# Optimization experiments

Measured on AMD Instinct MI355X. Metric: run time of the kernel, lower is better.

Reference implementation:

```python
import jax, jax.numpy as jnp
import numpy as np

N = 16384
IN_F = 256
OUT_F = 128
ALPHA = 0.2  # leaky relu negative slope
NEG = -9e15


def _xavier(key, shape, gain=1.414):
    fan_in, fan_out = shape
    a = gain * np.sqrt(6.0 / (fan_in + fan_out))
    return jax.random.uniform(key, shape, jnp.float32, -a, a)


def setup_inputs() -> dict:
    key = jax.random.key(0)
    k_h, k_adj, k_q, k_k, k_v = jax.random.split(key, 5)
    h = jax.random.normal(k_h, (N, IN_F), dtype=jnp.float32)
    adj = jax.random.randint(k_adj, (N, N), 0, 2, dtype=jnp.int32)
    W_query = _xavier(k_q, (IN_F, OUT_F))
    W_key = _xavier(k_k, (IN_F, OUT_F))
    W_value = _xavier(k_v, (IN_F, OUT_F))
    return {"h": h, "adj": adj, "W_query": W_query, "W_key": W_key, "W_value": W_value}


def reference(h, adj, W_query, W_key, W_value):
    # h: [N, in], adj: [N, N] 0/1
    Q = h @ W_query           # [N, out]
    K = h @ W_key             # [N, out]
    V = h @ W_value           # [N, out]
    e = jnp.einsum('nd,md->nm', Q, K)          # [N, N]
    e = jnp.where(e >= 0, e, ALPHA * e)         # leaky relu
    e = jnp.where(adj > 0, e, NEG)              # adjacency mask
    attention = jax.nn.softmax(e, axis=1)       # row softmax
    # dropout: eval mode (training=False) -> identity
    h_prime = attention @ V                     # [N, out]
    return jax.nn.elu(h_prime)                  # concat=True
```

## Files before the change

kernel.cpp:

```cpp
#include <hip/hip_runtime.h>

#define N_TOK 16384
#define ALPHA_LRELU 0.2f
#define NEGV -9e15f
#define NSPLIT 3
#define LOG2E 1.44269504f
#define DEFER_THR 8.0f

typedef _Float16 f16;
typedef __attribute__((ext_vector_type(8))) _Float16 f16x8;
typedef __attribute__((ext_vector_type(4))) float f32x4;
typedef __attribute__((ext_vector_type(4))) int i32x4;
typedef unsigned short u16;

__device__ __forceinline__ float bf2f(u16 b) {
  unsigned u = ((unsigned)b) << 16;
  return __builtin_bit_cast(float, u);
}
__device__ __forceinline__ f16x8 cvt8(i32x4 v) {
  f16x8 r;
#pragma unroll
  for (int i = 0; i < 4; ++i) {
    unsigned u = __builtin_bit_cast(unsigned, v[i]);
    r[2 * i]     = (f16)__builtin_bit_cast(float, (u & 0xffffu) << 16);
    r[2 * i + 1] = (f16)__builtin_bit_cast(float, u & 0xffff0000u);
  }
  return r;
}

__global__ __launch_bounds__(64) void detect_kernel(const u16* __restrict__ h16,
                                                    int* __restrict__ flag)
{
  int lane = threadIdx.x;
  unsigned u = h16[lane * 2];
  unsigned e = (u >> 7) & 0xFFu;
  int sane = (e >= 0x60u && e <= 0x8Eu) ? 1 : 0;
#pragma unroll
  for (int off = 32; off >= 1; off >>= 1) sane += __shfl_xor(sane, off);
  if (lane == 0) *flag = (sane >= 32) ? 1 : 0;
}

__global__ __launch_bounds__(256) void sentinel_kernel(float* __restrict__ out) {
  int i = blockIdx.x * 256 + threadIdx.x;
  if (i < N_TOK * 128) out[i] = 100.0f;
}

__global__ __launch_bounds__(256) void wt_kernel(
    const int* __restrict__ flag,
    const void* __restrict__ Wq, const void* __restrict__ Wk,
    const void* __restrict__ Wv, f16* __restrict__ Wt)
{
  const int isbf = *flag;
  int w = blockIdx.y;
  const void* W = (w == 0) ? Wq : (w == 1) ? Wk : Wv;
  int idx = blockIdx.x * 256 + threadIdx.x;
  int k = idx >> 7, n = idx & 127;
  float v = isbf ? bf2f(((const u16*)W)[idx]) : ((const float*)W)[idx];
  if (w == 0) v *= LOG2E;
  Wt[w * 32768 + n * 256 + k] = (f16)v;
}

__global__ __launch_bounds__(256) void qkv_kernel(
    const int* __restrict__ flag, const void* __restrict__ hvp,
    const f16* __restrict__ Wt,
    f16* __restrict__ Qo, f16* __restrict__ Ko, f16* __restrict__ Vt)
{
  const int isbf = *flag;
  const int mb = blockIdx.x * 64;
  const int gy = blockIdx.y;
  const int tid = threadIdx.x;
  const int wave = tid >> 6, lane = tid & 63, quad = lane >> 4, l16 = lane & 15;

  __shared__ __align__(16) f16 hs[64][256 + 8];

  if (isbf) {
    const u16* h = (const u16*)hvp;
#pragma unroll
    for (int i = 0; i < 8; ++i) {
      int c = i * 256 + tid;
      int r = c >> 5, o = c & 31;
      i32x4 v = *(const i32x4*)(h + (size_t)(mb + r) * 256 + o * 8);
      *(f16x8*)(&hs[r][o * 8]) = cvt8(v);
    }
  } else {
    const float* h = (const float*)hvp;
#pragma unroll
    for (int i = 0; i < 8; ++i) {
      int c = i * 256 + tid;
      int r = c >> 5, o = c & 31;
      const float* p = h + (size_t)(mb + r) * 256 + o * 8;
      f32x4 v0 = *(const f32x4*)p, v1 = *(const f32x4*)(p + 4);
      f16x8 q;
#pragma unroll
      for (int j = 0; j < 4; ++j) { q[j] = (f16)v0[j]; q[4 + j] = (f16)v1[j]; }
      *(f16x8*)(&hs[r][o * 8]) = q;
    }
  }
  __syncthreads();

  const f16* Wg = Wt + gy * 32768;

  if (gy < 2) {
    f16x8 a[8];
#pragma unroll
    for (int ks = 0; ks < 8; ++ks)
      a[ks] = *(const f16x8*)(&hs[wave * 16 + l16][ks * 32 + quad * 8]);
    f32x4 acc[8];
#pragma unroll
    for (int ct = 0; ct < 8; ++ct) acc[ct] = (f32x4){0.f, 0.f, 0.f, 0.f};
#pragma unroll
    for (int ks = 0; ks < 8; ++ks)
#pragma unroll
      for (int ct = 0; ct < 8; ++ct) {
        f16x8 b = *(const f16x8*)(Wg + (ct * 16 + l16) * 256 + ks * 32 + quad * 8);
        acc[ct] = __builtin_amdgcn_mfma_f32_16x16x32_f16(a[ks], b, acc[ct], 0, 0, 0);
      }
    f16* O = (gy == 0) ? Qo : Ko;
#pragma unroll
    for (int ct = 0; ct < 8; ++ct)
#pragma unroll
      for (int r = 0; r < 4; ++r)
        O[(size_t)(mb + wave * 16 + quad * 4 + r) * 128 + ct * 16 + l16] = (f16)acc[ct][r];
  } else {
    f32x4 acc[2][4];
#pragma unroll
    for (int ft = 0; ft < 2; ++ft)
#pragma unroll
      for (int bt = 0; bt < 4; ++bt) acc[ft][bt] = (f32x4){0.f, 0.f, 0.f, 0.f};
#pragma unroll
    for (int ks = 0; ks < 8; ++ks) {
      f16x8 a2[2], b2[4];
#pragma unroll
      for (int ft = 0; ft < 2; ++ft)
        a2[ft] = *(const f16x8*)(Wg + ((wave * 2 + ft) * 16 + l16) * 256 + ks * 32 + quad * 8);
#pragma unroll
      for (int bt = 0; bt < 4; ++bt)
        b2[bt] = *(const f16x8*)(&hs[bt * 16 + l16][ks * 32 + quad * 8]);
#pragma unroll
      for (int ft = 0; ft < 2; ++ft)
#pragma unroll
        for (int bt = 0; bt < 4; ++bt)
          acc[ft][bt] = __builtin_amdgcn_mfma_f32_16x16x32_f16(a2[ft], b2[bt], acc[ft][bt], 0, 0, 0);
    }
#pragma unroll
    for (int ft = 0; ft < 2; ++ft)
#pragma unroll
      for (int bt = 0; bt < 4; ++bt)
#pragma unroll
        for (int r = 0; r < 4; ++r)
          Vt[(size_t)((wave * 2 + ft) * 16 + quad * 4 + r) * N_TOK + mb + bt * 16 + l16] =
              (f16)acc[ft][bt][r];
  }
}

__global__ __launch_bounds__(256, 2) void flash_kernel(
    const f16* __restrict__ Q, const f16* __restrict__ Kg,
    const f16* __restrict__ Vt, const int* __restrict__ adj,
    float* __restrict__ Opart, float* __restrict__ mpart,
    float* __restrict__ lpart)
{
  const int qb = blockIdx.x * 64;
  const int ksec = blockIdx.y;
  const int base = 256 / NSPLIT;
  const int rem  = 256 % NSPLIT;
  const int iters = base + (ksec < rem ? 1 : 0);
  const int tile0 = ksec * base + (ksec < rem ? ksec : rem);
  const int kb0 = tile0 * 64;
  const int tid = threadIdx.x;
  const int wave = tid >> 6, lane = tid & 63, quad = lane >> 4, l16 = lane & 15;

  __shared__ __align__(16) f16 Ks[2][64][136];
  __shared__ __align__(16) f16 Vs[2][128][72];
  __shared__ __align__(16) f16 Ps[4][16][72];

  f16x8 qf[4];
#pragma unroll
  for (int ks = 0; ks < 4; ++ks)
    qf[ks] = *(const f16x8*)(Q + (size_t)(qb + wave * 16 + l16) * 128 + ks * 32 + quad * 8);

  f16x8 ONES;
#pragma unroll
  for (int j = 0; j < 8; ++j) ONES[j] = (f16)1.0f;

  const int* aprow[4];
#pragma unroll
  for (int r = 0; r < 4; ++r)
    aprow[r] = adj + (size_t)(qb + wave * 16 + quad * 4 + r) * N_TOK + l16;

  f32x4 Oacc[8];
#pragma unroll
  for (int ot = 0; ot < 8; ++ot) Oacc[ot] = (f32x4){0.f, 0.f, 0.f, 0.f};
  f32x4 Lacc = (f32x4){0.f, 0.f, 0.f, 0.f};
  float m2[4];
#pragma unroll
  for (int r = 0; r < 4; ++r) m2[r] = -INFINITY;

  i32x4 pK[4], pV[4];
  int am[4][4];

#pragma unroll
  for (int i = 0; i < 4; ++i) {
    int c = i * 256 + tid;
    pK[i] = *(const i32x4*)(Kg + (size_t)(kb0 + (c >> 4)) * 128 + (c & 15) * 8);
    pV[i] = *(const i32x4*)(Vt + (size_t)(c >> 3) * N_TOK + kb0 + (c & 7) * 8);
  }
#pragma unroll
  for (int r = 0; r < 4; ++r)
#pragma unroll
    for (int ct = 0; ct < 4; ++ct)
      am[r][ct] = aprow[r][kb0 + ct * 16];
#pragma unroll
  for (int i = 0; i < 4; ++i) {
    int c = i * 256 + tid;
    *(f16x8*)(&Ks[0][c >> 4][(c & 15) * 8]) = __builtin_bit_cast(f16x8, pK[i]);
    *(f16x8*)(&Vs[0][c >> 3][(c & 7) * 8])  = __builtin_bit_cast(f16x8, pV[i]);
  }
  if (iters > 1) {
    int kb = kb0 + 64;
#pragma unroll
    for (int i = 0; i < 4; ++i) {
      int c = i * 256 + tid;
      pK[i] = *(const i32x4*)(Kg + (size_t)(kb + (c >> 4)) * 128 + (c & 15) * 8);
      pV[i] = *(const i32x4*)(Vt + (size_t)(c >> 3) * N_TOK + kb + (c & 7) * 8);
    }
  }
  __syncthreads();

  for (int it = 0; it < iters; ++it) {
    const int cur = it & 1;
    const int nxt = cur ^ 1;

    if (it + 1 < iters) {
#pragma unroll
      for (int i = 0; i < 4; ++i) {
        int c = i * 256 + tid;
        *(f16x8*)(&Ks[nxt][c >> 4][(c & 15) * 8]) = __builtin_bit_cast(f16x8, pK[i]);
        *(f16x8*)(&Vs[nxt][c >> 3][(c & 7) * 8])  = __builtin_bit_cast(f16x8, pV[i]);
      }
    }
    if (it + 2 < iters) {
      int kb = kb0 + (it + 2) * 64;
#pragma unroll
      for (int i = 0; i < 4; ++i) {
        int c = i * 256 + tid;
        pK[i] = *(const i32x4*)(Kg + (size_t)(kb + (c >> 4)) * 128 + (c & 15) * 8);
        pV[i] = *(const i32x4*)(Vt + (size_t)(c >> 3) * N_TOK + kb + (c & 7) * 8);
      }
    }

    float sc[4][4];
#pragma unroll
    for (int ct = 0; ct < 4; ++ct) {
      f32x4 s = (f32x4){0.f, 0.f, 0.f, 0.f};
#pragma unroll
      for (int ks = 0; ks < 4; ++ks) {
        f16x8 b = *(const f16x8*)(&Ks[cur][ct * 16 + l16][ks * 32 + quad * 8]);
        s = __builtin_amdgcn_mfma_f32_16x16x32_f16(qf[ks], b, s, 0, 0, 0);
      }
#pragma unroll
      for (int r = 0; r < 4; ++r) {
        float v = s[r];
        v = fmaxf(v, ALPHA_LRELU * v);
        sc[ct][r] = (am[r][ct] > 0) ? v : NEGV;
      }
    }
    if (it + 1 < iters) {
      int kb = kb0 + (it + 1) * 64;
#pragma unroll
      for (int r = 0; r < 4; ++r)
#pragma unroll
        for (int ct = 0; ct < 4; ++ct)
          am[r][ct] = aprow[r][kb + ct * 16];
    }

    float mx[4];
#pragma unroll
    for (int r = 0; r < 4; ++r) {
      float m = fmaxf(fmaxf(sc[0][r], sc[1][r]), fmaxf(sc[2][r], sc[3][r]));
#pragma unroll
      for (int off = 8; off >= 1; off >>= 1)
        m = fmaxf(m, __shfl_xor(m, off, 16));
      mx[r] = m;
    }
    bool up = (mx[0] > m2[0] + DEFER_THR) | (mx[1] > m2[1] + DEFER_THR) |
              (mx[2] > m2[2] + DEFER_THR) | (mx[3] > m2[3] + DEFER_THR);
    if (__ballot(up)) {
      float al[4];
#pragma unroll
      for (int r = 0; r < 4; ++r) {
        float mn = fmaxf(m2[r], mx[r]);
        al[r] = exp2f(m2[r] - mn);
        m2[r] = mn;
      }
#pragma unroll
      for (int ot = 0; ot < 8; ++ot)
#pragma unroll
        for (int r = 0; r < 4; ++r) Oacc[ot][r] *= al[r];
#pragma unroll
      for (int r = 0; r < 4; ++r) Lacc[r] *= al[r];
    }

#pragma unroll
    for (int ct = 0; ct < 4; ++ct)
#pragma unroll
      for (int r = 0; r < 4; ++r)
        Ps[wave][quad * 4 + r][ct * 16 + l16] = (f16)exp2f(sc[ct][r] - m2[r]);

    asm volatile("s_waitcnt lgkmcnt(0)" ::: "memory");
    f16x8 pa0 = *(const f16x8*)(&Ps[wave][l16][quad * 8]);
    f16x8 pa1 = *(const f16x8*)(&Ps[wave][l16][32 + quad * 8]);
#pragma unroll
    for (int ot = 0; ot < 8; ++ot) {
      f16x8 b0 = *(const f16x8*)(&Vs[cur][ot * 16 + l16][quad * 8]);
      f16x8 b1 = *(const f16x8*)(&Vs[cur][ot * 16 + l16][32 + quad * 8]);
      Oacc[ot] = __builtin_amdgcn_mfma_f32_16x16x32_f16(pa0, b0, Oacc[ot], 0, 0, 0);
      Oacc[ot] = __builtin_amdgcn_mfma_f32_16x16x32_f16(pa1, b1, Oacc[ot], 0, 0, 0);
    }
    Lacc = __builtin_amdgcn_mfma_f32_16x16x32_f16(pa0, ONES, Lacc, 0, 0, 0);
    Lacc = __builtin_amdgcn_mfma_f32_16x16x32_f16(pa1, ONES, Lacc, 0, 0, 0);

    __syncthreads();
  }

  float* Op = Opart + (size_t)ksec * (N_TOK * 128);
#pragma unroll
  for (int ot = 0; ot < 8; ++ot)
#pragma unroll
    for (int r = 0; r < 4; ++r) {
      int row = qb + wave * 16 + quad * 4 + r;
      Op[(size_t)row * 128 + ot * 16 + l16] = Oacc[ot][r];
    }
  if (l16 == 0) {
#pragma unroll
    for (int r = 0; r < 4; ++r) {
      int row = qb + wave * 16 + quad * 4 + r;
      mpart[ksec * N_TOK + row] = m2[r];
      lpart[ksec * N_TOK + row] = Lacc[r];
    }
  }
}

__global__ __launch_bounds__(256) void combine_kernel(
    const float* __restrict__ Opart, const float* __restrict__ mpart,
    const float* __restrict__ lpart, float* __restrict__ out)
{
  const int qb = blockIdx.x * 64;
  const int t = threadIdx.x;
  __shared__ float sa[NSPLIT][64], sdn[64];
  if (t < 64) {
    float m = -INFINITY;
#pragma unroll
    for (int s = 0; s < NSPLIT; ++s) m = fmaxf(m, mpart[s * N_TOK + qb + t]);
    float dn = 0.f;
#pragma unroll
    for (int s = 0; s < NSPLIT; ++s) {
      float a = exp2f(mpart[s * N_TOK + qb + t] - m);
      sa[s][t] = a;
      dn += lpart[s * N_TOK + qb + t] * a;
    }
    sdn[t] = 1.0f / dn;
  }
  __syncthreads();
  float* Og = out + (size_t)qb * 128;
#pragma unroll
  for (int i = 0; i < 8; ++i) {
    int idx = (i * 256 + t) * 4;
    int row = idx >> 7;
    f32x4 acc = (f32x4){0.f, 0.f, 0.f, 0.f};
#pragma unroll
    for (int s = 0; s < NSPLIT; ++s) {
      f32x4 o = *(const f32x4*)(Opart + (size_t)s * (N_TOK * 128) + (size_t)qb * 128 + idx);
      float a = sa[s][row];
#pragma unroll
      for (int j = 0; j < 4; ++j) acc[j] += o[j] * a;
    }
    float dn = sdn[row];
    f32x4 v;
#pragma unroll
    for (int j = 0; j < 4; ++j) {
      float x = acc[j] * dn;
      v[j] = (x > 0.f) ? x : (__expf(x) - 1.f);
    }
    *(f32x4*)(Og + idx) = v;
  }
}

__global__ __launch_bounds__(256) void flash1_kernel(
    const f16* __restrict__ Q, const f16* __restrict__ Kg,
    const f16* __restrict__ Vt, const int* __restrict__ adj,
    float* __restrict__ out)
{
  const int qb = blockIdx.x * 64;
  const int tid = threadIdx.x;
  const int wave = tid >> 6, lane = tid & 63, quad = lane >> 4, l16 = lane & 15;

  __shared__ __align__(16) f16 Ks[64][136];
  __shared__ __align__(16) f16 Vs[128][72];
  __shared__ __align__(16) int As[64][68];
  __shared__ __align__(16) f16 Ps[4][16][72];

  f16x8 qf[4];
#pragma unroll
  for (int ks = 0; ks < 4; ++ks)
    qf[ks] = *(const f16x8*)(Q + (size_t)(qb + wave * 16 + l16) * 128 + ks * 32 + quad * 8);
  f16x8 ONES;
#pragma unroll
  for (int j = 0; j < 8; ++j) ONES[j] = (f16)1.0f;

  f32x4 Oacc[8];
#pragma unroll
  for (int ot = 0; ot < 8; ++ot) Oacc[ot] = (f32x4){0.f, 0.f, 0.f, 0.f};
  f32x4 Lacc = (f32x4){0.f, 0.f, 0.f, 0.f};
  float m2[4];
#pragma unroll
  for (int r = 0; r < 4; ++r) m2[r] = -INFINITY;

  i32x4 pK[4], pV[4], pA[4];
#pragma unroll
  for (int i = 0; i < 4; ++i) {
    int c = i * 256 + tid;
    pK[i] = *(const i32x4*)(Kg + (size_t)(c >> 4) * 128 + (c & 15) * 8);
    pV[i] = *(const i32x4*)(Vt + (size_t)(c >> 3) * N_TOK + (c & 7) * 8);
    pA[i] = *(const i32x4*)(adj + (size_t)(qb + (c >> 4)) * N_TOK + (c & 15) * 4);
  }

  for (int it = 0; it < 256; ++it) {
    __syncthreads();
#pragma unroll
    for (int i = 0; i < 4; ++i) {
      int c = i * 256 + tid;
      *(f16x8*)(&Ks[c >> 4][(c & 15) * 8]) = __builtin_bit_cast(f16x8, pK[i]);
      *(f16x8*)(&Vs[c >> 3][(c & 7) * 8])  = __builtin_bit_cast(f16x8, pV[i]);
      *(i32x4*)(&As[c >> 4][(c & 15) * 4]) = pA[i];
    }
    __syncthreads();
    if (it + 1 < 256) {
      int kb = (it + 1) * 64;
#pragma unroll
      for (int i = 0; i < 4; ++i) {
        int c = i * 256 + tid;
        pK[i] = *(const i32x4*)(Kg + (size_t)(kb + (c >> 4)) * 128 + (c & 15) * 8);
        pV[i] = *(const i32x4*)(Vt + (size_t)(c >> 3) * N_TOK + kb + (c & 7) * 8);
        pA[i] = *(const i32x4*)(adj + (size_t)(qb + (c >> 4)) * N_TOK + kb + (c & 15) * 4);
      }
    }
    float sc[4][4];
#pragma unroll
    for (int ct = 0; ct < 4; ++ct) {
      f32x4 s = (f32x4){0.f, 0.f, 0.f, 0.f};
#pragma unroll
      for (int ks = 0; ks < 4; ++ks) {
        f16x8 b = *(const f16x8*)(&Ks[ct * 16 + l16][ks * 32 + quad * 8]);
        s = __builtin_amdgcn_mfma_f32_16x16x32_f16(qf[ks], b, s, 0, 0, 0);
      }
#pragma unroll
      for (int r = 0; r < 4; ++r) {
        float v = s[r];
        v = fmaxf(v, ALPHA_LRELU * v);
        sc[ct][r] = (As[wave * 16 + quad * 4 + r][ct * 16 + l16] > 0) ? v : NEGV;
      }
    }
    float mx[4];
#pragma unroll
    for (int r = 0; r < 4; ++r) {
      float m = fmaxf(fmaxf(sc[0][r], sc[1][r]), fmaxf(sc[2][r], sc[3][r]));
#pragma unroll
      for (int off = 8; off >= 1; off >>= 1)
        m = fmaxf(m, __shfl_xor(m, off, 16));
      mx[r] = m;
    }
    bool up = (mx[0] > m2[0] + DEFER_THR) | (mx[1] > m2[1] + DEFER_THR) |
              (mx[2] > m2[2] + DEFER_THR) | (mx[3] > m2[3] + DEFER_THR);
    if (__ballot(up)) {
      float al[4];
#pragma unroll
      for (int r = 0; r < 4; ++r) {
        float mn = fmaxf(m2[r], mx[r]);
        al[r] = exp2f(m2[r] - mn);
        m2[r] = mn;
      }
#pragma unroll
      for (int ot = 0; ot < 8; ++ot)
#pragma unroll
        for (int r = 0; r < 4; ++r) Oacc[ot][r] *= al[r];
#pragma unroll
      for (int r = 0; r < 4; ++r) Lacc[r] *= al[r];
    }
#pragma unroll
    for (int ct = 0; ct < 4; ++ct)
#pragma unroll
      for (int r = 0; r < 4; ++r)
        Ps[wave][quad * 4 + r][ct * 16 + l16] = (f16)exp2f(sc[ct][r] - m2[r]);

    asm volatile("s_waitcnt lgkmcnt(0)" ::: "memory");
    f16x8 pa0 = *(const f16x8*)(&Ps[wave][l16][quad * 8]);
    f16x8 pa1 = *(const f16x8*)(&Ps[wave][l16][32 + quad * 8]);
#pragma unroll
    for (int ot = 0; ot < 8; ++ot) {
      f16x8 b0 = *(const f16x8*)(&Vs[ot * 16 + l16][quad * 8]);
      f16x8 b1 = *(const f16x8*)(&Vs[ot * 16 + l16][32 + quad * 8]);
      Oacc[ot] = __builtin_amdgcn_mfma_f32_16x16x32_f16(pa0, b0, Oacc[ot], 0, 0, 0);
      Oacc[ot] = __builtin_amdgcn_mfma_f32_16x16x32_f16(pa1, b1, Oacc[ot], 0, 0, 0);
    }
    Lacc = __builtin_amdgcn_mfma_f32_16x16x32_f16(pa0, ONES, Lacc, 0, 0, 0);
    Lacc = __builtin_amdgcn_mfma_f32_16x16x32_f16(pa1, ONES, Lacc, 0, 0, 0);
  }
#pragma unroll
  for (int ot = 0; ot < 8; ++ot)
#pragma unroll
    for (int r = 0; r < 4; ++r) {
      float v = Oacc[ot][r] / Lacc[r];
      v = (v > 0.f) ? v : (__expf(v) - 1.f);
      int row = qb + wave * 16 + quad * 4 + r;
      out[(size_t)row * 128 + ot * 16 + l16] = v;
    }
}

extern "C" void kernel_launch(void* const* d_in, const int* in_sizes, int n_in,
                              void* d_out, int out_size, void* d_ws, size_t ws_size,
                              hipStream_t stream)
{
  const void* h  = d_in[0];
  const int* adj = (const int*)d_in[1];
  const void* Wq = d_in[2];
  const void* Wk = d_in[3];
  const void* Wv = d_in[4];
  float* out = (float*)d_out;

  char* ws = (char*)d_ws;
  int* flag = (int*)ws;
  f16* Wt = (f16*)(ws + 1024);
  f16* Q  = (f16*)(ws + 262144);
  f16* K  = (f16*)(ws + 4456448);
  f16* Vt = (f16*)(ws + 8650752);
  float* Opart = (float*)(ws + 12845056);
  float* mpart = (float*)(ws + 38010880);
  float* lpart = (float*)(ws + 38207488);
  const size_t NEED_BASE  = 12845056;
  const size_t NEED_SPLIT = 38404096;

  if (ws_size < NEED_BASE) {
    sentinel_kernel<<<(N_TOK * 128 + 255) / 256, 256, 0, stream>>>(out);
    return;
  }

  detect_kernel<<<1, 64, 0, stream>>>((const u16*)h, flag);
  wt_kernel<<<dim3(128, 3), 256, 0, stream>>>(flag, Wq, Wk, Wv, Wt);
  qkv_kernel<<<dim3(256, 3), 256, 0, stream>>>(flag, h, Wt, Q, K, Vt);

  if (ws_size >= NEED_SPLIT) {
    flash_kernel<<<dim3(256, NSPLIT), 256, 0, stream>>>(Q, K, Vt, adj,
                                                        Opart, mpart, lpart);
    combine_kernel<<<dim3(256), 256, 0, stream>>>(Opart, mpart, lpart, out);
  } else {
    flash1_kernel<<<dim3(256), 256, 0, stream>>>(Q, K, Vt, adj, out);
  }
}
```

Baseline: 1.537 ms.

## Process two 16-row query tiles per wave and split keys four ways

Each wave now handles 32 query rows (two 16-row groups) against every K/V tile staged in shared memory. This halves K/V global and LDS traffic per query row and computes S transposed so each lane holds one query row. The adjacency mask is packed into bitmasks, and its loads are split so they interleave with the two PV passes. The key split goes from 3 to 4, giving 128x4 blocks with more accumulator registers per thread, which risks lower occupancy or spills.

```diff
diff --git a/kernel.cpp b/kernel.cpp
--- a/kernel.cpp
+++ b/kernel.cpp
@@ -3,11 +3,12 @@
 #define N_TOK 16384
 #define ALPHA_LRELU 0.2f
 #define NEGV -9e15f
-#define NSPLIT 3
+#define NSPLIT 4
 #define LOG2E 1.44269504f
 #define DEFER_THR 8.0f
 
 typedef _Float16 f16;
+typedef __attribute__((ext_vector_type(4))) _Float16 f16x4;
 typedef __attribute__((ext_vector_type(8))) _Float16 f16x8;
 typedef __attribute__((ext_vector_type(4))) float f32x4;
 typedef __attribute__((ext_vector_type(4))) int i32x4;
@@ -159,13 +160,10 @@
     float* __restrict__ Opart, float* __restrict__ mpart,
     float* __restrict__ lpart)
 {
-  const int qb = blockIdx.x * 64;
+  const int qb = blockIdx.x * 128;
   const int ksec = blockIdx.y;
-  const int base = 256 / NSPLIT;
-  const int rem  = 256 % NSPLIT;
-  const int iters = base + (ksec < rem ? 1 : 0);
-  const int tile0 = ksec * base + (ksec < rem ? ksec : rem);
-  const int kb0 = tile0 * 64;
+  const int iters = 256 / NSPLIT;
+  const int kb0 = ksec * iters * 64;
   const int tid = threadIdx.x;
   const int wave = tid >> 6, lane = tid & 63, quad = lane >> 4, l16 = lane & 15;
 
@@ -173,30 +171,33 @@
   __shared__ __align__(16) f16 Vs[2][128][72];
   __shared__ __align__(16) f16 Ps[4][16][72];
 
-  f16x8 qf[4];
-#pragma unroll
-  for (int ks = 0; ks < 4; ++ks)
-    qf[ks] = *(const f16x8*)(Q + (size_t)(qb + wave * 16 + l16) * 128 + ks * 32 + quad * 8);
+  f16x8 qfA[4], qfB[4];
+  const f16* qp = Q + (size_t)(qb + wave * 32 + l16) * 128;
+#pragma unroll
+  for (int ks = 0; ks < 4; ++ks) {
+    qfA[ks] = *(const f16x8*)(qp + ks * 32 + quad * 8);
+    qfB[ks] = *(const f16x8*)(qp + 16 * 128 + ks * 32 + quad * 8);
+  }
 
   f16x8 ONES;
 #pragma unroll
   for (int j = 0; j < 8; ++j) ONES[j] = (f16)1.0f;
 
-  const int* aprow[4];
-#pragma unroll
-  for (int r = 0; r < 4; ++r)
-    aprow[r] = adj + (size_t)(qb + wave * 16 + quad * 4 + r) * N_TOK + l16;
-
-  f32x4 Oacc[8];
-#pragma unroll
-  for (int ot = 0; ot < 8; ++ot) Oacc[ot] = (f32x4){0.f, 0.f, 0.f, 0.f};
-  f32x4 Lacc = (f32x4){0.f, 0.f, 0.f, 0.f};
-  float m2[4];
-#pragma unroll
-  for (int r = 0; r < 4; ++r) m2[r] = -INFINITY;
+  const int* aprA = adj + (size_t)(qb + wave * 32 + l16) * N_TOK;
+  const int* aprB = aprA + (size_t)16 * N_TOK;
+
+  f32x4 OA[8], OB[8];
+#pragma unroll
+  for (int ot = 0; ot < 8; ++ot) {
+    OA[ot] = (f32x4){0.f, 0.f, 0.f, 0.f};
+    OB[ot] = (f32x4){0.f, 0.f, 0.f, 0.f};
+  }
+  f32x4 LA = (f32x4){0.f, 0.f, 0.f, 0.f};
+  f32x4 LB = (f32x4){0.f, 0.f, 0.f, 0.f};
+  float mA = -INFINITY, mB = -INFINITY;
 
   i32x4 pK[4], pV[4];
-  int am[4][4];
+  unsigned amA, amB;
 
 #pragma unroll
   for (int i = 0; i < 4; ++i) {
@@ -204,11 +205,18 @@
     pK[i] = *(const i32x4*)(Kg + (size_t)(kb0 + (c >> 4)) * 128 + (c & 15) * 8);
     pV[i] = *(const i32x4*)(Vt + (size_t)(c >> 3) * N_TOK + kb0 + (c & 7) * 8);
   }
-#pragma unroll
-  for (int r = 0; r < 4; ++r)
+  {
+    unsigned a0 = 0, b0 = 0;
 #pragma unroll
     for (int ct = 0; ct < 4; ++ct)
-      am[r][ct] = aprow[r][kb0 + ct * 16];
+#pragma unroll
+      for (int r = 0; r < 4; ++r) {
+        int col = kb0 + ct * 16 + quad * 4 + r;
+        a0 |= (unsigned)(aprA[col] > 0) << (ct * 4 + r);
+        b0 |= (unsigned)(aprB[col] > 0) << (ct * 4 + r);
+      }
+    amA = a0; amB = b0;
+  }
 #pragma unroll
   for (int i = 0; i < 4; ++i) {
     int c = i * 256 + tid;
@@ -229,6 +237,7 @@
   for (int it = 0; it < iters; ++it) {
     const int cur = it & 1;
     const int nxt = cur ^ 1;
+    const int kbn = kb0 + (it + 1) * 64;
 
     if (it + 1 < iters) {
 #pragma unroll
@@ -248,94 +257,160 @@
       }
     }
 
-    float sc[4][4];
+    f32x4 sA[4], sB[4];
 #pragma unroll
     for (int ct = 0; ct < 4; ++ct) {
-      f32x4 s = (f32x4){0.f, 0.f, 0.f, 0.f};
+      sA[ct] = (f32x4){0.f, 0.f, 0.f, 0.f};
+      sB[ct] = (f32x4){0.f, 0.f, 0.f, 0.f};
+    }
+#pragma unroll
+    for (int ct = 0; ct < 4; ++ct)
 #pragma unroll
       for (int ks = 0; ks < 4; ++ks) {
-        f16x8 b = *(const f16x8*)(&Ks[cur][ct * 16 + l16][ks * 32 + quad * 8]);
-        s = __builtin_amdgcn_mfma_f32_16x16x32_f16(qf[ks], b, s, 0, 0, 0);
-      }
+        f16x8 a = *(const f16x8*)(&Ks[cur][ct * 16 + l16][ks * 32 + quad * 8]);
+        sA[ct] = __builtin_amdgcn_mfma_f32_16x16x32_f16(a, qfA[ks], sA[ct], 0, 0, 0);
+        sB[ct] = __builtin_amdgcn_mfma_f32_16x16x32_f16(a, qfB[ks], sB[ct], 0, 0, 0);
+      }
+
+    float scA[4][4], scB[4][4];
+#pragma unroll
+    for (int ct = 0; ct < 4; ++ct)
 #pragma unroll
       for (int r = 0; r < 4; ++r) {
-        float v = s[r];
-        v = fmaxf(v, ALPHA_LRELU * v);
-        sc[ct][r] = (am[r][ct] > 0) ? v : NEGV;
-      }
-    }
+        float vA = sA[ct][r];
+        vA = fmaxf(vA, ALPHA_LRELU * vA);
+        scA[ct][r] = ((amA >> (ct * 4 + r)) & 1u) ? vA : NEGV;
+        float vB = sB[ct][r];
+        vB = fmaxf(vB, ALPHA_LRELU * vB);
+        scB[ct][r] = ((amB >> (ct * 4 + r)) & 1u) ? vB : NEGV;
+      }
+
+    int tmA[16], tmB[16];
     if (it + 1 < iters) {
-      int kb = kb0 + (it + 1) * 64;
-#pragma unroll
-      for (int r = 0; r < 4; ++r)
-#pragma unroll
-        for (int ct = 0; ct < 4; ++ct)
-          am[r][ct] = aprow[r][kb + ct * 16];
-    }
-
-    float mx[4];
+#pragma unroll
+      for (int ct = 0; ct < 4; ++ct)
+#pragma unroll
+        for (int r = 0; r < 4; ++r)
+          tmA[ct * 4 + r] = aprA[kbn + ct * 16 + quad * 4 + r];
+    }
+
+    float mxA = scA[0][0], mxB = scB[0][0];
+#pragma unroll
+    for (int ct = 0; ct < 4; ++ct)
+#pragma unroll
+      for (int r = 0; r < 4; ++r) {
+        mxA = fmaxf(mxA, scA[ct][r]);
+        mxB = fmaxf(mxB, scB[ct][r]);
+      }
+    mxA = fmaxf(mxA, __shfl_xor(mxA, 16));
+    mxA = fmaxf(mxA, __shfl_xor(mxA, 32));
+    mxB = fmaxf(mxB, __shfl_xor(mxB, 16));
+    mxB = fmaxf(mxB, __shfl_xor(mxB, 32));
+
+    bool up = (mxA > mA + DEFER_THR) | (mxB > mB + DEFER_THR);
+    if (__ballot(up)) {
+      float mnA = fmaxf(mA, mxA), alA = exp2f(mA - mnA); mA = mnA;
+      float mnB = fmaxf(mB, mxB), alB = exp2f(mB - mnB); mB = mnB;
+      float aOA[4], aOB[4];
+#pragma unroll
+      for (int r = 0; r < 4; ++r) {
+        aOA[r] = __shfl(alA, quad * 4 + r);
+        aOB[r] = __shfl(alB, quad * 4 + r);
+      }
+#pragma unroll
+      for (int ot = 0; ot < 8; ++ot)
+#pragma unroll
+        for (int r = 0; r < 4; ++r) {
+          OA[ot][r] *= aOA[r];
+          OB[ot][r] *= aOB[r];
+        }
+#pragma unroll
+      for (int r = 0; r < 4; ++r) { LA[r] *= aOA[r]; LB[r] *= aOB[r]; }
+    }
+
+#pragma unroll
+    for (int ct = 0; ct < 4; ++ct) {
+      f16x4 pw;
+#pragma unroll
+      for (int r = 0; r < 4; ++r) pw[r] = (f16)exp2f(scA[ct][r] - mA);
+      *(f16x4*)(&Ps[wave][l16][ct * 16 + quad * 4]) = pw;
+    }
+    asm volatile("s_waitcnt lgkmcnt(0)" ::: "memory");
+    {
+      f16x8 pa0 = *(const f16x8*)(&Ps[wave][l16][quad * 8]);
+      f16x8 pa1 = *(const f16x8*)(&Ps[wave][l16][32 + quad * 8]);
+#pragma unroll
+      for (int ot = 0; ot < 8; ++ot) {
+        f16x8 b0 = *(const f16x8*)(&Vs[cur][ot * 16 + l16][quad * 8]);
+        f16x8 b1 = *(const f16x8*)(&Vs[cur][ot * 16 + l16][32 + quad * 8]);
+        OA[ot] = __builtin_amdgcn_mfma_f32_16x16x32_f16(pa0, b0, OA[ot], 0, 0, 0);
+        OA[ot] = __builtin_amdgcn_mfma_f32_16x16x32_f16(pa1, b1, OA[ot], 0, 0, 0);
+      }
+      LA = __builtin_amdgcn_mfma_f32_16x16x32_f16(pa0, ONES, LA, 0, 0, 0);
+      LA = __builtin_amdgcn_mfma_f32_16x16x32_f16(pa1, ONES, LA, 0, 0, 0);
+    }
+
+    if (it + 1 < iters) {
+#pragma unroll
+      for (int ct = 0; ct < 4; ++ct)
+#pragma unroll
+        for (int r = 0; r < 4; ++r)
+          tmB[ct * 4 + r] = aprB[kbn + ct * 16 + quad * 4 + r];
+    }
+
+#pragma unroll
+    for (int ct = 0; ct < 4; ++ct) {
+      f16x4 pw;
+#pragma unroll
+      for (int r = 0; r < 4; ++r) pw[r] = (f16)exp2f(scB[ct][r] - mB);
+      *(f16x4*)(&Ps[wave][l16][ct * 16 + quad * 4]) = pw;
+    }
+    asm volatile("s_waitcnt lgkmcnt(0)" ::: "memory");
+    {
+      f16x8 pa0 = *(const f16x8*)(&Ps[wave][l16][quad * 8]);
+      f16x8 pa1 = *(const f16x8*)(&Ps[wave][l16][32 + quad * 8]);
+#pragma unroll
+      for (int ot = 0; ot < 8; ++ot) {
+        f16x8 b0 = *(const f16x8*)(&Vs[cur][ot * 16 + l16][quad * 8]);
+        f16x8 b1 = *(const f16x8*)(&Vs[cur][ot * 16 + l16][32 + quad * 8]);
+        OB[ot] = __builtin_amdgcn_mfma_f32_16x16x32_f16(pa0, b0, OB[ot], 0, 0, 0);
+        OB[ot] = __builtin_amdgcn_mfma_f32_16x16x32_f16(pa1, b1, OB[ot], 0, 0, 0);
+      }
+      LB = __builtin_amdgcn_mfma_f32_16x16x32_f16(pa0, ONES, LB, 0, 0, 0);
+      LB = __builtin_amdgcn_mfma_f32_16x16x32_f16(pa1, ONES, LB, 0, 0, 0);
+    }
+
+    if (it + 1 < iters) {
+      unsigned a0 = 0, b0 = 0;
+#pragma unroll
+      for (int j = 0; j < 16; ++j) {
+        a0 |= (unsigned)(tmA[j] > 0) << j;
+        b0 |= (unsigned)(tmB[j] > 0) << j;
+      }
+      amA = a0; amB = b0;
+    }
+
+    __syncthreads();
+  }
+
+  float* Op = Opart + (size_t)ksec * (N_TOK * 128);
+#pragma unroll
+  for (int ot = 0; ot < 8; ++ot)
 #pragma unroll
     for (int r = 0; r < 4; ++r) {
-      float m = fmaxf(fmaxf(sc[0][r], sc[1][r]), fmaxf(sc[2][r], sc[3][r]));
-#pragma unroll
-      for (int off = 8; off >= 1; off >>= 1)
-        m = fmaxf(m, __shfl_xor(m, off, 16));
-      mx[r] = m;
-    }
-    bool up = (mx[0] > m2[0] + DEFER_THR) | (mx[1] > m2[1] + DEFER_THR) |
-              (mx[2] > m2[2] + DEFER_THR) | (mx[3] > m2[3] + DEFER_THR);
-    if (__ballot(up)) {
-      float al[4];
-#pragma unroll
-      for (int r = 0; r < 4; ++r) {
-        float mn = fmaxf(m2[r], mx[r]);
-        al[r] = exp2f(m2[r] - mn);
-        m2[r] = mn;
-      }
-#pragma unroll
-      for (int ot = 0; ot < 8; ++ot)
-#pragma unroll
-        for (int r = 0; r < 4; ++r) Oacc[ot][r] *= al[r];
-#pragma unroll
-      for (int r = 0; r < 4; ++r) Lacc[r] *= al[r];
-    }
-
-#pragma unroll
-    for (int ct = 0; ct < 4; ++ct)
-#pragma unroll
-      for (int r = 0; r < 4; ++r)
-        Ps[wave][quad * 4 + r][ct * 16 + l16] = (f16)exp2f(sc[ct][r] - m2[r]);
-
-    asm volatile("s_waitcnt lgkmcnt(0)" ::: "memory");
-    f16x8 pa0 = *(const f16x8*)(&Ps[wave][l16][quad * 8]);
-    f16x8 pa1 = *(const f16x8*)(&Ps[wave][l16][32 + quad * 8]);
-#pragma unroll
-    for (int ot = 0; ot < 8; ++ot) {
-      f16x8 b0 = *(const f16x8*)(&Vs[cur][ot * 16 + l16][quad * 8]);
-      f16x8 b1 = *(const f16x8*)(&Vs[cur][ot * 16 + l16][32 + quad * 8]);
-      Oacc[ot] = __builtin_amdgcn_mfma_f32_16x16x32_f16(pa0, b0, Oacc[ot], 0, 0, 0);
-      Oacc[ot] = __builtin_amdgcn_mfma_f32_16x16x32_f16(pa1, b1, Oacc[ot], 0, 0, 0);
-    }
-    Lacc = __builtin_amdgcn_mfma_f32_16x16x32_f16(pa0, ONES, Lacc, 0, 0, 0);
-    Lacc = __builtin_amdgcn_mfma_f32_16x16x32_f16(pa1, ONES, Lacc, 0, 0, 0);
-
-    __syncthreads();
-  }
-
-  float* Op = Opart + (size_t)ksec * (N_TOK * 128);
-#pragma unroll
-  for (int ot = 0; ot < 8; ++ot)
+      int rowA = qb + wave * 32 + quad * 4 + r;
+      Op[(size_t)rowA * 128 + ot * 16 + l16] = OA[ot][r];
+      Op[(size_t)(rowA + 16) * 128 + ot * 16 + l16] = OB[ot][r];
+    }
+  if (quad == 0) {
+    mpart[ksec * N_TOK + qb + wave * 32 + l16] = mA;
+    mpart[ksec * N_TOK + qb + wave * 32 + 16 + l16] = mB;
+  }
+  if (l16 == 0) {
 #pragma unroll
     for (int r = 0; r < 4; ++r) {
-      int row = qb + wave * 16 + quad * 4 + r;
-      Op[(size_t)row * 128 + ot * 16 + l16] = Oacc[ot][r];
-    }
-  if (l16 == 0) {
-#pragma unroll
-    for (int r = 0; r < 4; ++r) {
-      int row = qb + wave * 16 + quad * 4 + r;
-      mpart[ksec * N_TOK + row] = m2[r];
-      lpart[ksec * N_TOK + row] = Lacc[r];
+      lpart[ksec * N_TOK + qb + wave * 32 + quad * 4 + r] = LA[r];
+      lpart[ksec * N_TOK + qb + wave * 32 + 16 + quad * 4 + r] = LB[r];
     }
   }
 }
@@ -534,10 +609,10 @@
   f16* K  = (f16*)(ws + 4456448);
   f16* Vt = (f16*)(ws + 8650752);
   float* Opart = (float*)(ws + 12845056);
-  float* mpart = (float*)(ws + 38010880);
-  float* lpart = (float*)(ws + 38207488);
+  float* mpart = (float*)(ws + 46399488);
+  float* lpart = (float*)(ws + 46661632);
   const size_t NEED_BASE  = 12845056;
-  const size_t NEED_SPLIT = 38404096;
+  const size_t NEED_SPLIT = 46923776;
 
   if (ws_size < NEED_BASE) {
     sentinel_kernel<<<(N_TOK * 128 + 255) / 256, 256, 0, stream>>>(out);
@@ -549,7 +624,7 @@
   qkv_kernel<<<dim3(256, 3), 256, 0, stream>>>(flag, h, Wt, Q, K, Vt);
 
   if (ws_size >= NEED_SPLIT) {
-    flash_kernel<<<dim3(256, NSPLIT), 256, 0, stream>>>(Q, K, Vt, adj,
+    flash_kernel<<<dim3(128, NSPLIT), 256, 0, stream>>>(Q, K, Vt, adj,
                                                         Opart, mpart, lpart);
     combine_kernel<<<dim3(256), 256, 0, stream>>>(Opart, mpart, lpart, out);
   } else {
```

After: 1.531 ms. No clear change (-0.4%).

## Stage K/V tiles via direct global-to-LDS loads with XOR swizzle, single buffer

Applied to the files above, without the earlier changes.

Replaces register-staged double-buffered K/V tiles with global_load_lds direct-to-LDS transfers into a single buffer. Bank conflicts are avoided with an XOR swizzle instead of padding. The smaller LDS footprint and fewer registers allow raising the occupancy hint to 3 blocks per CU. The cost is that loads are no longer overlapped with compute inside a block: each iteration waits on vmcnt(0) with an extra barrier, so latency hiding depends on the other resident blocks.

```diff
diff --git a/kernel.cpp b/kernel.cpp
--- a/kernel.cpp
+++ b/kernel.cpp
@@ -26,6 +26,12 @@
     r[2 * i + 1] = (f16)__builtin_bit_cast(float, u & 0xffff0000u);
   }
   return r;
+}
+
+__device__ __forceinline__ void gload16(const void* g, void* l) {
+  __builtin_amdgcn_global_load_lds(
+      (const __attribute__((address_space(1))) unsigned*)g,
+      (__attribute__((address_space(3))) unsigned*)l, 16, 0, 0);
 }
 
 __global__ __launch_bounds__(64) void detect_kernel(const u16* __restrict__ h16,
@@ -153,7 +159,7 @@
   }
 }
 
-__global__ __launch_bounds__(256, 2) void flash_kernel(
+__global__ __launch_bounds__(256, 3) void flash_kernel(
     const f16* __restrict__ Q, const f16* __restrict__ Kg,
     const f16* __restrict__ Vt, const int* __restrict__ adj,
     float* __restrict__ Opart, float* __restrict__ mpart,
@@ -169,9 +175,11 @@
   const int tid = threadIdx.x;
   const int wave = tid >> 6, lane = tid & 63, quad = lane >> 4, l16 = lane & 15;
 
-  __shared__ __align__(16) f16 Ks[2][64][136];
-  __shared__ __align__(16) f16 Vs[2][128][72];
+  __shared__ __align__(16) f16 KsL[64 * 128];
+  __shared__ __align__(16) f16 VsL[128 * 64];
   __shared__ __align__(16) f16 Ps[4][16][72];
+
+  const int swl = (l16 & 7) << 4;
 
   f16x8 qf[4];
 #pragma unroll
@@ -195,66 +203,50 @@
 #pragma unroll
   for (int r = 0; r < 4; ++r) m2[r] = -INFINITY;
 
-  i32x4 pK[4], pV[4];
   int am[4][4];
 
-#pragma unroll
-  for (int i = 0; i < 4; ++i) {
-    int c = i * 256 + tid;
-    pK[i] = *(const i32x4*)(Kg + (size_t)(kb0 + (c >> 4)) * 128 + (c & 15) * 8);
-    pV[i] = *(const i32x4*)(Vt + (size_t)(c >> 3) * N_TOK + kb0 + (c & 7) * 8);
-  }
+  const char* Kc = (const char*)Kg;
+  const char* Vc = (const char*)Vt;
+  char* Kl = (char*)KsL;
+  char* Vl = (char*)VsL;
+
+#define STAGE_KV(KB)                                                          \
+  {                                                                           \
+    int kb_ = (KB);                                                           \
+    _Pragma("unroll")                                                         \
+    for (int i = 0; i < 4; ++i) {                                             \
+      int row = i * 16 + (tid >> 4);                                          \
+      int colb = ((tid & 15) * 16) ^ ((row & 7) << 4);                        \
+      gload16(Kc + (size_t)(kb_ + row) * 256 + colb,                          \
+              Kl + i * 4096 + wave * 1024);                                   \
+    }                                                                         \
+    _Pragma("unroll")                                                         \
+    for (int i = 0; i < 4; ++i) {                                             \
+      int d = i * 32 + (tid >> 3);                                            \
+      int colb = ((tid & 7) * 16) ^ ((d & 7) << 4);                           \
+      gload16(Vc + (size_t)d * (N_TOK * 2) + (size_t)kb_ * 2 + colb,          \
+              Vl + i * 4096 + wave * 1024);                                   \
+    }                                                                         \
+  }
+
+  STAGE_KV(kb0);
 #pragma unroll
   for (int r = 0; r < 4; ++r)
 #pragma unroll
     for (int ct = 0; ct < 4; ++ct)
       am[r][ct] = aprow[r][kb0 + ct * 16];
-#pragma unroll
-  for (int i = 0; i < 4; ++i) {
-    int c = i * 256 + tid;
-    *(f16x8*)(&Ks[0][c >> 4][(c & 15) * 8]) = __builtin_bit_cast(f16x8, pK[i]);
-    *(f16x8*)(&Vs[0][c >> 3][(c & 7) * 8])  = __builtin_bit_cast(f16x8, pV[i]);
-  }
-  if (iters > 1) {
-    int kb = kb0 + 64;
-#pragma unroll
-    for (int i = 0; i < 4; ++i) {
-      int c = i * 256 + tid;
-      pK[i] = *(const i32x4*)(Kg + (size_t)(kb + (c >> 4)) * 128 + (c & 15) * 8);
-      pV[i] = *(const i32x4*)(Vt + (size_t)(c >> 3) * N_TOK + kb + (c & 7) * 8);
-    }
-  }
+  asm volatile("s_waitcnt vmcnt(0)" ::: "memory");
   __syncthreads();
 
   for (int it = 0; it < iters; ++it) {
-    const int cur = it & 1;
-    const int nxt = cur ^ 1;
-
-    if (it + 1 < iters) {
-#pragma unroll
-      for (int i = 0; i < 4; ++i) {
-        int c = i * 256 + tid;
-        *(f16x8*)(&Ks[nxt][c >> 4][(c & 15) * 8]) = __builtin_bit_cast(f16x8, pK[i]);
-        *(f16x8*)(&Vs[nxt][c >> 3][(c & 7) * 8])  = __builtin_bit_cast(f16x8, pV[i]);
-      }
-    }
-    if (it + 2 < iters) {
-      int kb = kb0 + (it + 2) * 64;
-#pragma unroll
-      for (int i = 0; i < 4; ++i) {
-        int c = i * 256 + tid;
-        pK[i] = *(const i32x4*)(Kg + (size_t)(kb + (c >> 4)) * 128 + (c & 15) * 8);
-        pV[i] = *(const i32x4*)(Vt + (size_t)(c >> 3) * N_TOK + kb + (c & 7) * 8);
-      }
-    }
-
     float sc[4][4];
 #pragma unroll
     for (int ct = 0; ct < 4; ++ct) {
       f32x4 s = (f32x4){0.f, 0.f, 0.f, 0.f};
 #pragma unroll
       for (int ks = 0; ks < 4; ++ks) {
-        f16x8 b = *(const f16x8*)(&Ks[cur][ct * 16 + l16][ks * 32 + quad * 8]);
+        f16x8 b = *(const f16x8*)((const char*)KsL + (ct * 16 + l16) * 256 +
+                                  ((ks * 64 + quad * 16) ^ swl));
         s = __builtin_amdgcn_mfma_f32_16x16x32_f16(qf[ks], b, s, 0, 0, 0);
       }
 #pragma unroll
@@ -311,8 +303,9 @@
     f16x8 pa1 = *(const f16x8*)(&Ps[wave][l16][32 + quad * 8]);
 #pragma unroll
     for (int ot = 0; ot < 8; ++ot) {
-      f16x8 b0 = *(const f16x8*)(&Vs[cur][ot * 16 + l16][quad * 8]);
-      f16x8 b1 = *(const f16x8*)(&Vs[cur][ot * 16 + l16][32 + quad * 8]);
+      const char* vrow = (const char*)VsL + (ot * 16 + l16) * 128;
+      f16x8 b0 = *(const f16x8*)(vrow + ((quad * 16) ^ swl));
+      f16x8 b1 = *(const f16x8*)(vrow + ((64 + quad * 16) ^ swl));
       Oacc[ot] = __builtin_amdgcn_mfma_f32_16x16x32_f16(pa0, b0, Oacc[ot], 0, 0, 0);
       Oacc[ot] = __builtin_amdgcn_mfma_f32_16x16x32_f16(pa1, b1, Oacc[ot], 0, 0, 0);
     }
@@ -320,7 +313,13 @@
     Lacc = __builtin_amdgcn_mfma_f32_16x16x32_f16(pa1, ONES, Lacc, 0, 0, 0);
 
     __syncthreads();
-  }
+    if (it + 1 < iters) {
+      STAGE_KV(kb0 + (it + 1) * 64);
+    }
+    asm volatile("s_waitcnt vmcnt(0)" ::: "memory");
+    __syncthreads();
+  }
+#undef STAGE_KV
 
   float* Op = Opart + (size_t)ksec * (N_TOK * 128);
 #pragma unroll
```

Result: faster. 1.490 ms (-3.1%).
